# Optimization experiments

Hardware: AMD Instinct MI355X
Metric: run time of the kernel (lower is better)

## Reference

```python
import jax, jax.numpy as jnp
import numpy as np

HEAD_DIM = 128
NUM_HEADS = 16
HIDDEN = 2048
SEQ = 4096
ROPE_THETA = 10000.0
RMS_EPS = 1e-6


def _rms_norm(x, w, eps=RMS_EPS):
    # per-head RMSNorm over last dim (head_dim)
    var = jnp.mean(jnp.square(x), axis=-1, keepdims=True)
    return x * jax.lax.rsqrt(var + eps) * w


def _rope_cos_sin(position_ids, dim=HEAD_DIM, theta=ROPE_THETA):
    freqs = 1.0 / theta ** (jnp.arange(0, dim, 2, dtype=jnp.float32) / dim)  # [dim/2]
    ang = position_ids.astype(jnp.float32)[:, None] * freqs[None, :]  # [S, dim/2]
    return jnp.cos(ang), jnp.sin(ang)


def _apply_rope(x, cos, sin):
    # x: [S, H, D]; pairs (x0, x1) along last dim act as complex numbers
    S, H, D = x.shape
    xr = x.astype(jnp.float32).reshape(S, H, D // 2, 2)
    x0, x1 = xr[..., 0], xr[..., 1]
    c = cos[:, None, :]  # [S, 1, D/2]
    s = sin[:, None, :]
    o0 = x0 * c - x1 * s
    o1 = x0 * s + x1 * c
    out = jnp.stack((o0, o1), axis=-1).reshape(S, H, D)
    return out.astype(x.dtype)


def setup_inputs() -> dict:
    key = jax.random.key(0)
    ks = jax.random.split(key, 8)
    std = 0.02
    return {
        "hidden_states": jax.random.normal(ks[0], (SEQ, HIDDEN), dtype=jnp.float32),
        "position_ids": jnp.arange(SEQ, dtype=jnp.int64 if jax.config.jax_enable_x64 else jnp.int32),
        "wq": jax.random.normal(ks[1], (HIDDEN, HIDDEN), dtype=jnp.float32) * std,
        "wk": jax.random.normal(ks[2], (HIDDEN, HIDDEN), dtype=jnp.float32) * std,
        "wv": jax.random.normal(ks[3], (HIDDEN, HIDDEN), dtype=jnp.float32) * std,
        "wo": jax.random.normal(ks[4], (HIDDEN, HIDDEN), dtype=jnp.float32) * std,
        "q_norm_w": jnp.ones((HEAD_DIM,), dtype=jnp.float32),
        "k_norm_w": jnp.ones((HEAD_DIM,), dtype=jnp.float32),
    }


def reference(hidden_states, position_ids, wq, wk, wv, wo, q_norm_w, k_norm_w):
    S = hidden_states.shape[0]
    # QKV projections (NormalLinear: x @ weight)
    xq = hidden_states @ wq
    xk = hidden_states @ wk
    xv = hidden_states @ wv
    # split heads: [S, H, D]
    xq = xq.reshape(S, NUM_HEADS, HEAD_DIM)
    xk = xk.reshape(S, NUM_HEADS, HEAD_DIM)
    xv = xv.reshape(S, NUM_HEADS, HEAD_DIM)
    # per-head qk RMSNorm
    xq = _rms_norm(xq, q_norm_w)
    xk = _rms_norm(xk, k_norm_w)
    # rotary embedding
    cos, sin = _rope_cos_sin(position_ids)
    xq = _apply_rope(xq, cos, sin)
    xk = _apply_rope(xk, cos, sin)
    # scaled dot-product attention (no mask), TNH layout
    context = jax.nn.dot_product_attention(xq, xk, xv)
    # merge heads and output projection (dropout p=0 -> identity)
    out = context.reshape(S, NUM_HEADS * HEAD_DIM) @ wo
    return out
```

## Files before the change

### kernel.cpp

```cpp
#include <hip/hip_runtime.h>

typedef __bf16 bf16x8 __attribute__((ext_vector_type(8)));
typedef __bf16 bf16x4 __attribute__((ext_vector_type(4)));
typedef float  f32x4  __attribute__((ext_vector_type(4)));

#define MFMA16(A, B, C) __builtin_amdgcn_mfma_f32_16x16x32_bf16(A, B, C, 0, 0, 0)
#define AS1 __attribute__((address_space(1)))
#define AS3 __attribute__((address_space(3)))

#if __has_builtin(__builtin_amdgcn_exp2f)
#define EXP2F(x) __builtin_amdgcn_exp2f(x)
#else
#define EXP2F(x) exp2f(x)
#endif

__global__ __launch_bounds__(256) void convert_f32_bf16(const float* __restrict__ src,
                                                        __bf16* __restrict__ dst) {
    size_t i = ((size_t)blockIdx.x * 256 + threadIdx.x) * 4;
    float4 v = *(const float4*)(src + i);
    bf16x4 o;
    o.x = (__bf16)v.x; o.y = (__bf16)v.y; o.z = (__bf16)v.z; o.w = (__bf16)v.w;
    *(bf16x4*)(dst + i) = o;
}

__global__ __launch_bounds__(256) void transpose_conv(const float* __restrict__ src,
                                                      __bf16* __restrict__ dst) {
    __shared__ float t[32][33];
    int x0 = blockIdx.x * 32, y0 = blockIdx.y * 32;
    int tx = threadIdx.x, ty = threadIdx.y;
    for (int r = 0; r < 4; ++r)
        t[ty + 8 * r][tx] = src[(size_t)(y0 + ty + 8 * r) * 2048 + x0 + tx];
    __syncthreads();
    for (int r = 0; r < 4; ++r)
        dst[(size_t)(x0 + ty + 8 * r) * 2048 + y0 + tx] = (__bf16)t[tx][ty + 8 * r];
}

__global__ __launch_bounds__(256) void v_transpose(const __bf16* __restrict__ qkv,
                                                   __bf16* __restrict__ vtb) {
    __shared__ __bf16 t[32][33];
    int h = blockIdx.z;
    int s0 = blockIdx.x * 32, d0 = blockIdx.y * 32;
    int tx = threadIdx.x, ty = threadIdx.y;
    for (int r = 0; r < 4; ++r)
        t[ty + 8 * r][tx] = qkv[(size_t)(s0 + ty + 8 * r) * 6144 + 4096 + h * 128 + d0 + tx];
    __syncthreads();
    for (int r = 0; r < 4; ++r)
        vtb[(size_t)h * 128 * 4096 + (size_t)(d0 + ty + 8 * r) * 4096 + s0 + tx] = t[tx][ty + 8 * r];
}

__global__ __launch_bounds__(64) void rmsrope(const __bf16* __restrict__ qkv,
                                              const float* __restrict__ qw,
                                              const float* __restrict__ kw,
                                              const int* __restrict__ pos_ids,
                                              __bf16* __restrict__ qhb,
                                              __bf16* __restrict__ khb) {
    int s = blockIdx.x;
    int slot = blockIdx.y;
    int lane = threadIdx.x;
    bool isQ = slot < 16;
    int h = slot & 15;
    size_t base = (size_t)s * 6144 + (isQ ? 0 : 2048) + h * 128 + lane * 2;
    float x0 = (float)qkv[base], x1 = (float)qkv[base + 1];
    float ss = x0 * x0 + x1 * x1;
    for (int m = 1; m < 64; m <<= 1) ss += __shfl_xor(ss, m);
    float rr = rsqrtf(ss * (1.0f / 128.0f) + 1e-6f);
    const float* wp = isQ ? qw : kw;
    float n0 = x0 * rr * wp[lane * 2], n1 = x1 * rr * wp[lane * 2 + 1];
    float freq = powf(10000.0f, -(float)lane * (1.0f / 64.0f));
    float ang = (float)pos_ids[s] * freq;
    float sn, cs;
    sincosf(ang, &sn, &cs);
    float o0 = n0 * cs - n1 * sn;
    float o1 = n0 * sn + n1 * cs;
    if (isQ) { o0 *= 0.12751744416196178f; o1 *= 0.12751744416196178f; }
    __bf16* dst = (isQ ? qhb : khb) + (size_t)h * 4096 * 128 + (size_t)s * 128 + lane * 2;
    dst[0] = (__bf16)o0; dst[1] = (__bf16)o1;
}

template <bool F32OUT>
__global__ __launch_bounds__(256) void gemm_bt(const __bf16* __restrict__ A, int lda,
                                               const __bf16* __restrict__ Bt, int ldb,
                                               void* __restrict__ Cout, int ldc, int K) {
    __shared__ __bf16 as[128][32];
    __shared__ __bf16 bs[128][32];
    const int m0 = blockIdx.x * 128, n0 = blockIdx.y * 128;
    const int t = threadIdx.x;
    const int lane = t & 63, w = t >> 6;
    const int wm = (w >> 1) * 64, wn = (w & 1) * 64;
    const int ln = lane & 15, quad = lane >> 4;
    auto as3 = (AS3 uint32_t*)as;
    auto bs3 = (AS3 uint32_t*)bs;
    f32x4 acc[4][4] = {};
    for (int k0 = 0; k0 < K; k0 += 32) {
        for (int c = 0; c < 2; ++c) {
            int g = c * 256 + t;
            int row = g >> 2, kc = g & 3;
            const __bf16* ga = &A[(size_t)(m0 + row) * lda + k0 + kc * 8];
            const __bf16* gb = &Bt[(size_t)(n0 + row) * ldb + k0 + kc * 8];
            __builtin_amdgcn_global_load_lds((const AS1 uint32_t*)ga,
                                             as3 + c * 1024 + w * 256, 16, 0, 0);
            __builtin_amdgcn_global_load_lds((const AS1 uint32_t*)gb,
                                             bs3 + c * 1024 + w * 256, 16, 0, 0);
        }
        __syncthreads();
        bf16x8 af[4], bfr[4];
        for (int i = 0; i < 4; ++i) af[i] = *(const bf16x8*)&as[wm + i * 16 + ln][quad * 8];
        for (int j = 0; j < 4; ++j) bfr[j] = *(const bf16x8*)&bs[wn + j * 16 + ln][quad * 8];
        for (int i = 0; i < 4; ++i)
            for (int j = 0; j < 4; ++j)
                acc[i][j] = MFMA16(af[i], bfr[j], acc[i][j]);
        __syncthreads();
    }
    for (int i = 0; i < 4; ++i)
        for (int j = 0; j < 4; ++j)
            for (int r = 0; r < 4; ++r) {
                int row = m0 + wm + i * 16 + quad * 4 + r;
                int col = n0 + wn + j * 16 + ln;
                if (F32OUT) ((float*)Cout)[(size_t)row * ldc + col] = acc[i][j][r];
                else        ((__bf16*)Cout)[(size_t)row * ldc + col] = (__bf16)acc[i][j][r];
            }
}

__global__ __launch_bounds__(256) void flash_attn(const __bf16* __restrict__ Q,
                                                  const __bf16* __restrict__ Kb,
                                                  const __bf16* __restrict__ Vt,
                                                  __bf16* __restrict__ ctx) {
    __shared__ __bf16 kbuf[2][64][128];
    __shared__ __bf16 vbuf[2][128][64];
    __shared__ __bf16 ps[4][32][64];

    int bid = blockIdx.x + (int)gridDim.x * blockIdx.y;
    int swz = (bid & 7) * 64 + (bid >> 3);
    const int h  = swz >> 5;
    const int m0 = (swz & 31) * 128;

    const int t = threadIdx.x;
    const int lane = t & 63, w = t >> 6;
    const int ln = lane & 15, quad = lane >> 4;
    const __bf16* Qh = Q + (size_t)h * 4096 * 128;
    const __bf16* Kh = Kb + (size_t)h * 4096 * 128;
    const __bf16* Vh = Vt + (size_t)h * 128 * 4096;

    const int kcc = (t & 15) ^ ((t >> 4) & 7);
    const int vcc = (t & 7) ^ ((t >> 3) & 7);
    auto kb3 = (AS3 uint32_t*)&kbuf[0][0][0];
    auto vb3 = (AS3 uint32_t*)&vbuf[0][0][0];
    const char* kbase = (const char*)&kbuf[0][0][0];
    const char* vbase = (const char*)&vbuf[0][0][0];

    bf16x8 qf[2][4];
    for (int half = 0; half < 2; ++half) {
        for (int i = 0; i < 4; ++i) {
            int row = (t >> 4) + i * 16;
            *(uint4*)&kbuf[0][row][(t & 15) * 8] =
                *(const uint4*)&Qh[(size_t)(m0 + half * 64 + row) * 128 + kcc * 8];
        }
        __syncthreads();
        int r = w * 16 + ln;
        for (int kk = 0; kk < 4; ++kk)
            qf[half][kk] = *(const bf16x8*)(kbase + r * 256 + ((((kk * 4 + quad) ^ (ln & 7)) << 4)));
        __syncthreads();
    }

#define STAGE_KV(buf, tile)                                                          \
    for (int i = 0; i < 4; ++i) {                                                    \
        int krow = (t >> 4) + i * 16;                                                \
        __builtin_amdgcn_global_load_lds(                                            \
            (const AS1 uint32_t*)&Kh[(size_t)((tile) * 64 + krow) * 128 + kcc * 8],  \
            kb3 + (buf) * 4096 + (w * 64 + i * 256) * 4, 16, 0, 0);                  \
        int vrow = (t >> 3) + i * 32;                                                \
        __builtin_amdgcn_global_load_lds(                                            \
            (const AS1 uint32_t*)&Vh[(size_t)vrow * 4096 + (tile) * 64 + vcc * 8],   \
            vb3 + (buf) * 4096 + (w * 64 + i * 256) * 4, 16, 0, 0);                  \
    }

    STAGE_KV(0, 0)
    __syncthreads();

    f32x4 oacc[2][8] = {};
    float rs[2][4] = {};
    int cur = 0;

    for (int kb = 0; kb < 64; ++kb) {
        if (kb + 1 < 64) { STAGE_KV(cur ^ 1, kb + 1) }

        const char* ksb = kbase + cur * 16384;
        const char* vsb = vbase + cur * 16384;

        f32x4 sacc[2][4];
        const f32x4 mC = {-16.5f, -16.5f, -16.5f, -16.5f};
        for (int i = 0; i < 2; ++i)
            for (int j = 0; j < 4; ++j) sacc[i][j] = mC;
        for (int j = 0; j < 4; ++j)
            for (int kk = 0; kk < 4; ++kk) {
                bf16x8 kf = *(const bf16x8*)(ksb + (j * 16 + ln) * 256 +
                                             (((kk * 4 + quad) ^ (ln & 7)) << 4));
                sacc[0][j] = MFMA16(qf[0][kk], kf, sacc[0][j]);
                sacc[1][j] = MFMA16(qf[1][kk], kf, sacc[1][j]);
            }

        for (int i = 0; i < 2; ++i)
            for (int j = 0; j < 4; ++j)
                for (int r = 0; r < 4; ++r) {
                    float p = EXP2F(sacc[i][j][r]);
                    rs[i][r] += p;
                    int prow = i * 16 + quad * 4 + r;
                    ps[w][prow][(j * 16 + ln) ^ ((prow & 7) << 3)] = (__bf16)p;
                }

        bf16x8 pf[2][2];
        for (int i = 0; i < 2; ++i)
            for (int kk = 0; kk < 2; ++kk)
                pf[i][kk] = *(const bf16x8*)&ps[w][i * 16 + ln][(kk * 32 + quad * 8) ^ ((ln & 7) << 3)];
        for (int t8 = 0; t8 < 8; ++t8)
            for (int kk = 0; kk < 2; ++kk) {
                bf16x8 vf = *(const bf16x8*)(vsb + (t8 * 16 + ln) * 128 +
                                             (((kk * 4 + quad) ^ (ln & 7)) << 4));
                oacc[0][t8] = MFMA16(pf[0][kk], vf, oacc[0][t8]);
                oacc[1][t8] = MFMA16(pf[1][kk], vf, oacc[1][t8]);
            }
        __syncthreads();
        cur ^= 1;
    }
#undef STAGE_KV

    float inv[2][4];
    for (int i = 0; i < 2; ++i)
        for (int r = 0; r < 4; ++r) {
            float s = rs[i][r];
            for (int msk = 1; msk < 16; msk <<= 1) s += __shfl_xor(s, msk);
            inv[i][r] = 1.0f / s;
        }
    for (int i = 0; i < 2; ++i)
        for (int t8 = 0; t8 < 8; ++t8)
            for (int r = 0; r < 4; ++r) {
                int row = m0 + i * 64 + w * 16 + quad * 4 + r;
                int col = h * 128 + t8 * 16 + ln;
                ctx[(size_t)row * 2048 + col] = (__bf16)(oacc[i][t8][r] * inv[i][r]);
            }
}

extern "C" void kernel_launch(void* const* d_in, const int* in_sizes, int n_in,
                              void* d_out, int out_size, void* d_ws, size_t ws_size,
                              hipStream_t stream) {
    const float* hs  = (const float*)d_in[0];
    const int*   pos = (const int*)d_in[1];
    const float* wq  = (const float*)d_in[2];
    const float* wk  = (const float*)d_in[3];
    const float* wv  = (const float*)d_in[4];
    const float* wo  = (const float*)d_in[5];
    const float* qw  = (const float*)d_in[6];
    const float* kw  = (const float*)d_in[7];

    char* ws = (char*)d_ws;
    const size_t MB = 1024 * 1024;
    __bf16* xb     = (__bf16*)(ws + 0);
    __bf16* wqkvtb = (__bf16*)(ws + 16 * MB);
    __bf16* qhb    = (__bf16*)(ws + 0);
    __bf16* khb    = (__bf16*)(ws + 16 * MB);
    __bf16* vtb    = (__bf16*)(ws + 32 * MB);
    __bf16* qkvb   = (__bf16*)(ws + 48 * MB);
    __bf16* ctxb   = (__bf16*)(ws + 48 * MB);
    __bf16* wotb   = (__bf16*)(ws + 96 * MB);

    dim3 tb(32, 8);
    convert_f32_bf16<<<8192, 256, 0, stream>>>(hs, xb);
    transpose_conv<<<dim3(64, 64), tb, 0, stream>>>(wq, wqkvtb);
    transpose_conv<<<dim3(64, 64), tb, 0, stream>>>(wk, wqkvtb + (size_t)2048 * 2048);
    transpose_conv<<<dim3(64, 64), tb, 0, stream>>>(wv, wqkvtb + (size_t)2 * 2048 * 2048);
    transpose_conv<<<dim3(64, 64), tb, 0, stream>>>(wo, wotb);

    gemm_bt<false><<<dim3(32, 48), 256, 0, stream>>>(xb, 2048, wqkvtb, 2048, qkvb, 6144, 2048);

    rmsrope<<<dim3(4096, 32), 64, 0, stream>>>(qkvb, qw, kw, pos, qhb, khb);
    v_transpose<<<dim3(128, 4, 16), tb, 0, stream>>>(qkvb, vtb);

    flash_attn<<<dim3(32, 16), 256, 0, stream>>>(qhb, khb, vtb, ctxb);

    gemm_bt<true><<<dim3(32, 16), 256, 0, stream>>>(ctxb, 2048, wotb, 2048, d_out, 2048, 2048);
}
```

Baseline: 539.8 us.

## Triple-buffer GEMM LDS tiles with prefetch two stages ahead

The bf16 GEMM kernel now keeps three LDS buffers for the A and B tiles and issues global-to-LDS loads two K-steps ahead. It waits on partial vmcnt counts and raw barriers instead of a full __syncthreads, so memory latency can overlap with the MFMA work. This triples the GEMM's LDS use, which may lower occupancy, and correctness depends on the hand-written waitcnt counts.

```diff
diff --git a/kernel.cpp b/kernel.cpp
--- a/kernel.cpp
+++ b/kernel.cpp
@@ -81,36 +81,54 @@
 __global__ __launch_bounds__(256) void gemm_bt(const __bf16* __restrict__ A, int lda,
                                                const __bf16* __restrict__ Bt, int ldb,
                                                void* __restrict__ Cout, int ldc, int K) {
-    __shared__ __bf16 as[128][32];
-    __shared__ __bf16 bs[128][32];
+    __shared__ __bf16 as[3][128][32];
+    __shared__ __bf16 bs[3][128][32];
     const int m0 = blockIdx.x * 128, n0 = blockIdx.y * 128;
     const int t = threadIdx.x;
     const int lane = t & 63, w = t >> 6;
     const int wm = (w >> 1) * 64, wn = (w & 1) * 64;
     const int ln = lane & 15, quad = lane >> 4;
-    auto as3 = (AS3 uint32_t*)as;
-    auto bs3 = (AS3 uint32_t*)bs;
+    auto as3 = (AS3 uint32_t*)&as[0][0][0];
+    auto bs3 = (AS3 uint32_t*)&bs[0][0][0];
     f32x4 acc[4][4] = {};
-    for (int k0 = 0; k0 < K; k0 += 32) {
-        for (int c = 0; c < 2; ++c) {
-            int g = c * 256 + t;
-            int row = g >> 2, kc = g & 3;
-            const __bf16* ga = &A[(size_t)(m0 + row) * lda + k0 + kc * 8];
-            const __bf16* gb = &Bt[(size_t)(n0 + row) * ldb + k0 + kc * 8];
-            __builtin_amdgcn_global_load_lds((const AS1 uint32_t*)ga,
-                                             as3 + c * 1024 + w * 256, 16, 0, 0);
-            __builtin_amdgcn_global_load_lds((const AS1 uint32_t*)gb,
-                                             bs3 + c * 1024 + w * 256, 16, 0, 0);
+
+#define G_STAGE(buf, k0)                                                             \
+    for (int c = 0; c < 2; ++c) {                                                    \
+        int g = c * 256 + t;                                                         \
+        int row = g >> 2, kc = g & 3;                                                \
+        __builtin_amdgcn_global_load_lds(                                            \
+            (const AS1 uint32_t*)&A[(size_t)(m0 + row) * lda + (k0) + kc * 8],       \
+            as3 + (buf) * 2048 + c * 1024 + w * 256, 16, 0, 0);                      \
+        __builtin_amdgcn_global_load_lds(                                            \
+            (const AS1 uint32_t*)&Bt[(size_t)(n0 + row) * ldb + (k0) + kc * 8],      \
+            bs3 + (buf) * 2048 + c * 1024 + w * 256, 16, 0, 0);                      \
+    }
+
+    const int nk = K >> 5;
+    G_STAGE(0, 0)
+    G_STAGE(1, 32)
+    for (int kt = 0; kt < nk; ++kt) {
+        const int nxt = kt + 2;
+        if (nxt < nk) {
+            G_STAGE(nxt % 3, nxt * 32)
+            asm volatile("s_waitcnt vmcnt(8)" ::: "memory");
+        } else if (nxt == nk) {
+            asm volatile("s_waitcnt vmcnt(4)" ::: "memory");
+        } else {
+            asm volatile("s_waitcnt vmcnt(0)" ::: "memory");
         }
-        __syncthreads();
+        __builtin_amdgcn_s_barrier();
+        const int b = kt % 3;
         bf16x8 af[4], bfr[4];
-        for (int i = 0; i < 4; ++i) af[i] = *(const bf16x8*)&as[wm + i * 16 + ln][quad * 8];
-        for (int j = 0; j < 4; ++j) bfr[j] = *(const bf16x8*)&bs[wn + j * 16 + ln][quad * 8];
+        for (int i = 0; i < 4; ++i) af[i] = *(const bf16x8*)&as[b][wm + i * 16 + ln][quad * 8];
+        for (int j = 0; j < 4; ++j) bfr[j] = *(const bf16x8*)&bs[b][wn + j * 16 + ln][quad * 8];
         for (int i = 0; i < 4; ++i)
             for (int j = 0; j < 4; ++j)
                 acc[i][j] = MFMA16(af[i], bfr[j], acc[i][j]);
-        __syncthreads();
-    }
+        __builtin_amdgcn_s_barrier();
+    }
+#undef G_STAGE
+
     for (int i = 0; i < 4; ++i)
         for (int j = 0; j < 4; ++j)
             for (int r = 0; r < 4; ++r) {
```

Result: faster. 515.1 us (-4.6%).
